# Kernel optimization log

Hardware: AMD Instinct MI355X
Metric: run time of the kernel (lower is better)

Reference implementation:

```python
import jax, jax.numpy as jnp
import numpy as np

EMBED_DIM = 768
NUM_HEADS = 12
HEAD_DIM = EMBED_DIM // NUM_HEADS
SCALE = HEAD_DIM ** -0.5


def setup_inputs() -> dict:
    key = jax.random.key(0)
    k1, k2, k3, k4, k5 = jax.random.split(key, 5)
    B, T = 8, 1024
    init = 0.02
    return {
        "hidden_states": jax.random.normal(k1, (B, T, EMBED_DIM), dtype=jnp.float32),
        "qkv_w": jax.random.normal(k2, (EMBED_DIM, 3 * EMBED_DIM), dtype=jnp.float32) * init,
        "qkv_b": jnp.zeros((3 * EMBED_DIM,), dtype=jnp.float32),
        "proj_w": jax.random.normal(k3, (EMBED_DIM, EMBED_DIM), dtype=jnp.float32) * init,
        "proj_b": jnp.zeros((EMBED_DIM,), dtype=jnp.float32),
    }


def reference(hidden_states, qkv_w, qkv_b, proj_w, proj_b):
    B, T, E = hidden_states.shape
    # fused QKV projection: [B, T, 3E] -> [3, B, H, T, Dh]
    mixed = hidden_states @ qkv_w + qkv_b
    mixed = mixed.reshape(B, T, 3, NUM_HEADS, HEAD_DIM).transpose(2, 0, 3, 1, 4)
    q, k, v = mixed[0], mixed[1], mixed[2]
    # scores: [B, H, T, T]
    scores = jnp.einsum("bhqd,bhkd->bhqk", q, k) * SCALE
    probs = jax.nn.softmax(scores, axis=-1)
    # context: [B, T, H, Dh] -> [B, T, E]
    ctx = jnp.einsum("bhqk,bhkd->bqhd", probs, v).reshape(B, T, E)
    return ctx @ proj_w + proj_b
```

## Files before the change

### kernel.cpp

```cpp
#include <hip/hip_runtime.h>
#include <hip/hip_bf16.h>

#define B_ 8
#define T_ 1024
#define E_ 768
#define H_ 12
#define DH_ 64
#define E3_ 2304
#define M_ (B_ * T_)
#define SCALE_LOG2E 0.18033688011112042f

typedef __attribute__((ext_vector_type(8))) short short8;
typedef __attribute__((ext_vector_type(4))) float float4_;
typedef __attribute__((ext_vector_type(4))) unsigned short ushort4_;

__device__ __forceinline__ unsigned short f2bf(float f) {
    union { float f; unsigned int u; } v; v.f = f;
    unsigned int r = v.u + 0x7fffu + ((v.u >> 16) & 1u);
    return (unsigned short)(r >> 16);
}

__device__ __forceinline__ void gld_lds16(const unsigned short* g, unsigned short* l) {
    __builtin_amdgcn_global_load_lds(
        (const __attribute__((address_space(1))) void*)g,
        (__attribute__((address_space(3))) void*)l,
        16, 0, 0);
}

__global__ __launch_bounds__(256) void prep(const float* __restrict__ hs,
                                            const float* __restrict__ qkv_w,
                                            const float* __restrict__ proj_w,
                                            unsigned short* __restrict__ hs_bf,
                                            unsigned short* __restrict__ qkvwT,
                                            unsigned short* __restrict__ projwT) {
    __shared__ float tile[32][33];
    const int id = blockIdx.x;
    const int tid = threadIdx.x;
    if (id < 6144) {
        const int i = (id * 256 + tid) * 4;
        float4_ v = *(const float4_*)(hs + i);
        ushort4_ o;
        o.x = f2bf(v.x); o.y = f2bf(v.y); o.z = f2bf(v.z); o.w = f2bf(v.w);
        *(ushort4_*)(hs_bf + i) = o;
        return;
    }
    const float* W; unsigned short* Wt; int N, bx, by;
    if (id < 6144 + 1728) {
        const int t = id - 6144; W = qkv_w; Wt = qkvwT; N = E3_;
        bx = t % 72; by = t / 72;
    } else {
        const int t = id - 7872; W = proj_w; Wt = projwT; N = E_;
        bx = t % 24; by = t / 24;
    }
    const int k0 = by * 32, n0 = bx * 32;
    const int tx = tid & 31, ty = tid >> 5;
    for (int i = ty; i < 32; i += 8)
        tile[i][tx] = W[(size_t)(k0 + i) * N + n0 + tx];
    __syncthreads();
    for (int i = ty; i < 32; i += 8)
        Wt[(size_t)(n0 + i) * E_ + k0 + tx] = f2bf(tile[tx][i]);
}

template <int STORE_MODE>
__global__ __launch_bounds__(256) void gemm_mfma(const unsigned short* __restrict__ A,
                                                 const unsigned short* __restrict__ Wt,
                                                 const float* __restrict__ bias,
                                                 void* __restrict__ Cout,
                                                 unsigned short* __restrict__ Vt,
                                                 int M, int N, int K) {
    __shared__ __align__(16) unsigned short Al[2][128 * 32];
    __shared__ __align__(16) unsigned short Wl[2][128 * 32];

    const int tid = threadIdx.x;
    const int lane = tid & 63;
    const int w = tid >> 6;

    const int id = blockIdx.x;
    const int xcd = id & 7;
    const int slot = id >> 3;
    const int bx = slot >> 3;
    const int by = xcd * 8 + (slot & 7);
    const int bm = by * 128;
    const int bn = bx * 128;

    const int wm = (w >> 1) * 64;
    const int wn = (w & 1) * 64;
    const int quad = lane >> 4;
    const int l16 = lane & 15;

    const int srow = w * 32 + (lane >> 2);
    const int schunk = (lane & 3) * 8;
    const int sbase = w * 32 * 32 + lane * 8;

    const unsigned short* ga = A + (size_t)(bm + srow) * K + schunk;
    const unsigned short* gw = Wt + (size_t)(bn + srow) * K + schunk;

    float4_ acc[4][4] = {};

    gld_lds16(ga, &Al[0][sbase]);
    gld_lds16(ga + (size_t)16 * K, &Al[0][sbase + 512]);
    gld_lds16(gw, &Wl[0][sbase]);
    gld_lds16(gw + (size_t)16 * K, &Wl[0][sbase + 512]);

    const int NI = K >> 5;
    for (int i = 0; i < NI; ++i) {
        const int cur = i & 1;
        __syncthreads();
        if (i + 1 < NI) {
            const unsigned short* ga2 = ga + (size_t)(i + 1) * 32;
            const unsigned short* gw2 = gw + (size_t)(i + 1) * 32;
            const int nxt = cur ^ 1;
            gld_lds16(ga2, &Al[nxt][sbase]);
            gld_lds16(ga2 + (size_t)16 * K, &Al[nxt][sbase + 512]);
            gld_lds16(gw2, &Wl[nxt][sbase]);
            gld_lds16(gw2 + (size_t)16 * K, &Wl[nxt][sbase + 512]);
        }
        short8 af[4], bf[4];
#pragma unroll
        for (int mt = 0; mt < 4; ++mt)
            af[mt] = *(const short8*)(&Al[cur][(wm + mt * 16 + l16) * 32 + quad * 8]);
#pragma unroll
        for (int nt = 0; nt < 4; ++nt)
            bf[nt] = *(const short8*)(&Wl[cur][(wn + nt * 16 + l16) * 32 + quad * 8]);
#pragma unroll
        for (int mt = 0; mt < 4; ++mt)
#pragma unroll
            for (int nt = 0; nt < 4; ++nt)
                acc[mt][nt] = __builtin_amdgcn_mfma_f32_16x16x32_bf16(af[mt], bf[nt],
                                                                      acc[mt][nt], 0, 0, 0);
    }

    if (STORE_MODE == 2 && bn >= 1536) {
        const int b = bm >> 10;
        const int tloc = (bm & 1023) + wm;
#pragma unroll
        for (int nt = 0; nt < 4; ++nt) {
            const int col = bn + wn + nt * 16 + l16;
            const int n = col - 1536;
            const int h = n >> 6, d = n & 63;
            const float bv = bias[col];
            const size_t vrow = (size_t)((b * H_ + h) * 64 + d) * T_;
#pragma unroll
            for (int mt = 0; mt < 4; ++mt) {
                ushort4_ pk;
                pk.x = f2bf(acc[mt][nt][0] + bv);
                pk.y = f2bf(acc[mt][nt][1] + bv);
                pk.z = f2bf(acc[mt][nt][2] + bv);
                pk.w = f2bf(acc[mt][nt][3] + bv);
                *(ushort4_*)(Vt + vrow + tloc + mt * 16 + quad * 4) = pk;
            }
        }
    } else {
        const float qs = (STORE_MODE == 2 && bn < 768) ? SCALE_LOG2E : 1.0f;
#pragma unroll
        for (int nt = 0; nt < 4; ++nt) {
            const int col = bn + wn + nt * 16 + l16;
            const float bv = bias[col];
#pragma unroll
            for (int mt = 0; mt < 4; ++mt) {
#pragma unroll
                for (int i = 0; i < 4; ++i) {
                    const int row = bm + wm + mt * 16 + quad * 4 + i;
                    const float v = (acc[mt][nt][i] + bv) * qs;
                    if (STORE_MODE >= 1)
                        ((unsigned short*)Cout)[(size_t)row * N + col] = f2bf(v);
                    else
                        ((float*)Cout)[(size_t)row * N + col] = v;
                }
            }
        }
    }
}

__global__ __launch_bounds__(256) void attn_mfma(const unsigned short* __restrict__ mixed,
                                                 const unsigned short* __restrict__ Vt,
                                                 unsigned short* __restrict__ ctx) {
    const int bh = blockIdx.x;
    const int b = bh / H_;
    const int h = bh % H_;
    const int q0 = blockIdx.y * 128;
    const int tid = threadIdx.x;
    const int lane = tid & 63;
    const int w = tid >> 6;
    const int quad = lane >> 4;
    const int l16 = lane & 15;

    __shared__ __align__(16) unsigned short Kl[8 * 520];
    __shared__ __align__(16) unsigned short Vl[8 * 520];
    __shared__ __align__(16) unsigned short Pl[4][32 * 72];
    unsigned short* pw = &Pl[w][0];

    short8 qf[2][2];
#pragma unroll
    for (int hh = 0; hh < 2; ++hh) {
        const size_t qrow = (size_t)(b * T_ + q0 + w * 32 + hh * 16 + l16) * E3_ + h * 64;
        qf[hh][0] = *(const short8*)(mixed + qrow + quad * 8);
        qf[hh][1] = *(const short8*)(mixed + qrow + 32 + quad * 8);
    }

    float4_ o[2][4] = {};
    float lps[2] = {0.0f, 0.0f};

    const size_t kbase = (size_t)(b * T_) * E3_ + E_ + h * 64;
    const size_t vtb = (size_t)bh * 64 * T_;

    const int srow = tid >> 3;
    const int sc = tid & 7;

    for (int kv0 = 0; kv0 < T_; kv0 += 64) {
        short8 k1 = *(const short8*)(mixed + kbase + (size_t)(kv0 + srow) * E3_ + sc * 8);
        short8 k2 = *(const short8*)(mixed + kbase + (size_t)(kv0 + srow + 32) * E3_ + sc * 8);
        short8 v1 = *(const short8*)(Vt + vtb + (size_t)srow * T_ + kv0 + sc * 8);
        short8 v2 = *(const short8*)(Vt + vtb + (size_t)(srow + 32) * T_ + kv0 + sc * 8);
        __syncthreads();
        *(short8*)(&Kl[sc * 520 + srow * 8]) = k1;
        *(short8*)(&Kl[sc * 520 + (srow + 32) * 8]) = k2;
        *(short8*)(&Vl[sc * 520 + srow * 8]) = v1;
        *(short8*)(&Vl[sc * 520 + (srow + 32) * 8]) = v2;
        __syncthreads();

        float4_ st[2][4];
#pragma unroll
        for (int nt = 0; nt < 4; ++nt) {
            const int key = nt * 16 + l16;
            short8 kf0 = *(const short8*)(&Kl[quad * 520 + key * 8]);
            short8 kf1 = *(const short8*)(&Kl[(4 + quad) * 520 + key * 8]);
#pragma unroll
            for (int hh = 0; hh < 2; ++hh) {
                float4_ z = {};
                z = __builtin_amdgcn_mfma_f32_16x16x32_bf16(kf0, qf[hh][0], z, 0, 0, 0);
                st[hh][nt] = __builtin_amdgcn_mfma_f32_16x16x32_bf16(kf1, qf[hh][1], z, 0, 0, 0);
            }
        }

#pragma unroll
        for (int hh = 0; hh < 2; ++hh) {
#pragma unroll
            for (int nt = 0; nt < 4; ++nt) {
                ushort4_ pk;
                float p0 = exp2f(st[hh][nt][0]);
                float p1 = exp2f(st[hh][nt][1]);
                float p2 = exp2f(st[hh][nt][2]);
                float p3 = exp2f(st[hh][nt][3]);
                pk.x = f2bf(p0); pk.y = f2bf(p1); pk.z = f2bf(p2); pk.w = f2bf(p3);
                lps[hh] += (p0 + p1) + (p2 + p3);
                *(ushort4_*)(&pw[(hh * 16 + l16) * 72 + nt * 16 + quad * 4]) = pk;
            }
        }

        short8 pf[2][2];
#pragma unroll
        for (int hh = 0; hh < 2; ++hh) {
            pf[hh][0] = *(const short8*)(&pw[(hh * 16 + l16) * 72 + quad * 8]);
            pf[hh][1] = *(const short8*)(&pw[(hh * 16 + l16) * 72 + 32 + quad * 8]);
        }

#pragma unroll
        for (int dt = 0; dt < 4; ++dt) {
            const int d = dt * 16 + l16;
            short8 vf0 = *(const short8*)(&Vl[quad * 520 + d * 8]);
            short8 vf1 = *(const short8*)(&Vl[(4 + quad) * 520 + d * 8]);
#pragma unroll
            for (int hh = 0; hh < 2; ++hh) {
                o[hh][dt] = __builtin_amdgcn_mfma_f32_16x16x32_bf16(pf[hh][0], vf0, o[hh][dt], 0, 0, 0);
                o[hh][dt] = __builtin_amdgcn_mfma_f32_16x16x32_bf16(pf[hh][1], vf1, o[hh][dt], 0, 0, 0);
            }
        }
    }

#pragma unroll
    for (int hh = 0; hh < 2; ++hh) {
        float l = lps[hh];
        l += __shfl_xor(l, 16, 64);
        l += __shfl_xor(l, 32, 64);
        float4_ inv;
#pragma unroll
        for (int i = 0; i < 4; ++i)
            inv[i] = 1.0f / __shfl(l, quad * 4 + i, 16);
#pragma unroll
        for (int dt = 0; dt < 4; ++dt) {
#pragma unroll
            for (int i = 0; i < 4; ++i) {
                const float v = o[hh][dt][i] * inv[i];
                const size_t row = (size_t)(b * T_ + q0 + w * 32 + hh * 16 + quad * 4 + i);
                ctx[row * E_ + h * 64 + dt * 16 + l16] = f2bf(v);
            }
        }
    }
}

extern "C" void kernel_launch(void* const* d_in, const int* in_sizes, int n_in,
                              void* d_out, int out_size, void* d_ws, size_t ws_size,
                              hipStream_t stream) {
    const float* hs     = (const float*)d_in[0];
    const float* qkv_w  = (const float*)d_in[1];
    const float* qkv_b  = (const float*)d_in[2];
    const float* proj_w = (const float*)d_in[3];
    const float* proj_b = (const float*)d_in[4];
    float* out = (float*)d_out;

    unsigned short* hs_bf  = (unsigned short*)d_ws;
    unsigned short* qkvwT  = hs_bf + (size_t)M_ * E_;
    unsigned short* projwT = qkvwT + (size_t)E3_ * E_;
    unsigned short* mixed  = projwT + (size_t)E_ * E_;
    unsigned short* Vt     = mixed + (size_t)M_ * E3_;
    unsigned short* ctx    = hs_bf;

    prep<<<8448, 256, 0, stream>>>(hs, qkv_w, proj_w, hs_bf, qkvwT, projwT);

    gemm_mfma<2><<<(E3_ / 128) * (M_ / 128), 256, 0, stream>>>(hs_bf, qkvwT, qkv_b,
                                                               (void*)mixed, Vt, M_, E3_, E_);
    attn_mfma<<<dim3(B_ * H_, T_ / 128), 256, 0, stream>>>(mixed, Vt, ctx);
    gemm_mfma<0><<<(E_ / 128) * (M_ / 128), 256, 0, stream>>>(ctx, projwT, proj_b,
                                                              (void*)out, nullptr, M_, E_, E_);
}
```

Before: 214.8 us.

## Add 256x256-tile pipelined MFMA GEMM for the QKV projection

```diff
diff --git a/kernel.cpp b/kernel.cpp
--- a/kernel.cpp
+++ b/kernel.cpp
@@ -130,38 +130,186 @@
                                                                       acc[mt][nt], 0, 0, 0);
     }
 
+    {
+        const float qs = 1.0f;
+#pragma unroll
+        for (int nt = 0; nt < 4; ++nt) {
+            const int col = bn + wn + nt * 16 + l16;
+            const float bv = bias[col];
+#pragma unroll
+            for (int mt = 0; mt < 4; ++mt) {
+#pragma unroll
+                for (int i = 0; i < 4; ++i) {
+                    const int row = bm + wm + mt * 16 + quad * 4 + i;
+                    const float v = (acc[mt][nt][i] + bv) * qs;
+                    if (STORE_MODE >= 1)
+                        ((unsigned short*)Cout)[(size_t)row * N + col] = f2bf(v);
+                    else
+                        ((float*)Cout)[(size_t)row * N + col] = v;
+                }
+            }
+        }
+    }
+    (void)Vt;
+}
+
+template <int STORE_MODE>
+__global__ __launch_bounds__(512, 2) void gemm256(const unsigned short* __restrict__ A,
+                                                  const unsigned short* __restrict__ Wt,
+                                                  const float* __restrict__ bias,
+                                                  void* __restrict__ Cout,
+                                                  unsigned short* __restrict__ Vt,
+                                                  int M, int N, int K) {
+    __shared__ __align__(16) unsigned short lds[65536];
+
+    const int tid = threadIdx.x;
+    const int lane = tid & 63;
+    const int w = tid >> 6;
+    const int quad = lane >> 4;
+    const int l16 = lane & 15;
+
+    const int id = blockIdx.x;
+    const int xcd = id & 7;
+    const int slot = id >> 3;
+    const int bx = slot >> 2;
+    const int byl = slot & 3;
+    const int bm = (xcd * 4 + byl) * 256;
+    const int bn = bx * 256;
+
+    const int rb = tid >> 3;
+    const int csw = (((tid & 7) ^ (rb & 7)) << 3);
+    const unsigned short* ga = A + (size_t)(bm + rb) * K + csw;
+    const unsigned short* gb = Wt + (size_t)(bn + (rb & 31) + ((rb >> 5) & 1) * 64) * K + csw;
+    unsigned short* ldst = lds + tid * 8;
+
+#define STA(p, h, s, kt) gld_lds16(ga + ((size_t)((h) * 128 + (s) * 64) * K + (kt) * 64), \
+                                   ldst + ((p) * 2 + (h)) * 8192 + (s) * 4096)
+#define STB(p, h, s, kt) gld_lds16(gb + ((size_t)((h) * 128 + (s) * 32) * K + (kt) * 64), \
+                                   ldst + 32768 + ((p) * 2 + (h)) * 8192 + (s) * 4096)
+
+    const int sw0 = ((quad ^ (l16 & 7)) << 3);
+    const int sw1 = (((quad + 4) ^ (l16 & 7)) << 3);
+    const unsigned short* rdA = lds + (w >> 2) * 8192 + l16 * 64;
+    const unsigned short* rdB = lds + 32768 + ((w & 3) >> 1) * 8192 + ((w & 1) * 32 + l16) * 64;
+
+    short8 aF[4][2], bF0[2][2], bF1[2][2];
+    float4_ acc[8][4] = {};
+
+#define LDA(p, mh) { \
+    const unsigned short* _a = rdA + (p) * 16384 + (mh) * 4096; \
+    _Pragma("unroll") for (int mt = 0; mt < 4; ++mt) { \
+        aF[mt][0] = *(const short8*)(_a + mt * 1024 + sw0); \
+        aF[mt][1] = *(const short8*)(_a + mt * 1024 + sw1); } }
+#define LDB(dst, p, nh) { \
+    const unsigned short* _b = rdB + (p) * 16384 + (nh) * 4096; \
+    dst[0][0] = *(const short8*)(_b + sw0); \
+    dst[0][1] = *(const short8*)(_b + sw1); \
+    dst[1][0] = *(const short8*)(_b + 1024 + sw0); \
+    dst[1][1] = *(const short8*)(_b + 1024 + sw1); }
+
+#define MMA(mh, nh, BF) \
+    __builtin_amdgcn_s_barrier(); \
+    asm volatile("s_waitcnt lgkmcnt(0)" ::: "memory"); \
+    __builtin_amdgcn_sched_barrier(0); \
+    __builtin_amdgcn_s_setprio(1); \
+    _Pragma("unroll") for (int mt = 0; mt < 4; ++mt) \
+    _Pragma("unroll") for (int nt = 0; nt < 2; ++nt) { \
+        acc[(mh) * 4 + mt][(nh) * 2 + nt] = __builtin_amdgcn_mfma_f32_16x16x32_bf16( \
+            aF[mt][0], BF[nt][0], acc[(mh) * 4 + mt][(nh) * 2 + nt], 0, 0, 0); \
+        acc[(mh) * 4 + mt][(nh) * 2 + nt] = __builtin_amdgcn_mfma_f32_16x16x32_bf16( \
+            aF[mt][1], BF[nt][1], acc[(mh) * 4 + mt][(nh) * 2 + nt], 0, 0, 0); } \
+    __builtin_amdgcn_s_setprio(0);
+
+#define WAITV8 asm volatile("s_waitcnt vmcnt(8)" ::: "memory"); __builtin_amdgcn_s_barrier();
+
+    STA(0, 0, 0, 0); STA(0, 1, 0, 0);
+    STB(0, 0, 0, 0); STB(0, 1, 0, 0);
+    STB(0, 0, 1, 0); STB(0, 1, 1, 0);
+    STA(0, 0, 1, 0); STA(0, 1, 1, 0);
+    STA(1, 0, 0, 1); STA(1, 1, 0, 1);
+    STB(1, 0, 0, 1); STB(1, 1, 0, 1);
+    STB(1, 0, 1, 1); STB(1, 1, 1, 1);
+    asm volatile("s_waitcnt vmcnt(6)" ::: "memory");
+    __builtin_amdgcn_s_barrier();
+
+    const int NJ = K >> 7;
+#pragma unroll 1
+    for (int j = 0; j < NJ; ++j) {
+        const int t1 = 2 * j + 1, t2 = 2 * j + 2, t3 = 2 * j + 3;
+        const bool st = (j < NJ - 1);
+
+        LDA(0, 0); LDB(bF0, 0, 0);
+        STA(1, 0, 1, t1); STA(1, 1, 1, t1);
+        MMA(0, 0, bF0);
+        WAITV8;
+        LDB(bF1, 0, 1);
+        if (st) { STA(0, 0, 0, t2); STA(0, 1, 0, t2); }
+        MMA(0, 1, bF1);
+        WAITV8;
+        LDA(0, 1);
+        if (st) { STB(0, 0, 0, t2); STB(0, 1, 0, t2); }
+        MMA(1, 0, bF0);
+        WAITV8;
+        if (st) { STB(0, 0, 1, t2); STB(0, 1, 1, t2); }
+        MMA(1, 1, bF1);
+        if (j == NJ - 1) asm volatile("s_waitcnt vmcnt(0)" ::: "memory");
+        else             asm volatile("s_waitcnt vmcnt(8)" ::: "memory");
+        __builtin_amdgcn_s_barrier();
+        LDA(1, 0); LDB(bF0, 1, 0);
+        if (st) { STA(0, 0, 1, t2); STA(0, 1, 1, t2); }
+        MMA(0, 0, bF0);
+        WAITV8;
+        LDB(bF1, 1, 1);
+        if (st) { STA(1, 0, 0, t3); STA(1, 1, 0, t3); }
+        MMA(0, 1, bF1);
+        WAITV8;
+        LDA(1, 1);
+        if (st) { STB(1, 0, 0, t3); STB(1, 1, 0, t3); }
+        MMA(1, 0, bF0);
+        WAITV8;
+        if (st) { STB(1, 0, 1, t3); STB(1, 1, 1, t3); }
+        MMA(1, 1, bF1);
+        WAITV8;
+    }
+#undef STA
+#undef STB
+#undef LDA
+#undef LDB
+#undef MMA
+#undef WAITV8
+
     if (STORE_MODE == 2 && bn >= 1536) {
         const int b = bm >> 10;
-        const int tloc = (bm & 1023) + wm;
-#pragma unroll
-        for (int nt = 0; nt < 4; ++nt) {
-            const int col = bn + wn + nt * 16 + l16;
+        const int tloc = (bm & 1023) + (w >> 2) * 128;
+#pragma unroll
+        for (int ni = 0; ni < 4; ++ni) {
+            const int col = bn + (w & 3) * 64 + (ni >> 1) * 32 + (ni & 1) * 16 + l16;
             const int n = col - 1536;
             const int h = n >> 6, d = n & 63;
             const float bv = bias[col];
             const size_t vrow = (size_t)((b * H_ + h) * 64 + d) * T_;
 #pragma unroll
-            for (int mt = 0; mt < 4; ++mt) {
+            for (int mi = 0; mi < 8; ++mi) {
                 ushort4_ pk;
-                pk.x = f2bf(acc[mt][nt][0] + bv);
-                pk.y = f2bf(acc[mt][nt][1] + bv);
-                pk.z = f2bf(acc[mt][nt][2] + bv);
-                pk.w = f2bf(acc[mt][nt][3] + bv);
-                *(ushort4_*)(Vt + vrow + tloc + mt * 16 + quad * 4) = pk;
+                pk.x = f2bf(acc[mi][ni][0] + bv);
+                pk.y = f2bf(acc[mi][ni][1] + bv);
+                pk.z = f2bf(acc[mi][ni][2] + bv);
+                pk.w = f2bf(acc[mi][ni][3] + bv);
+                *(ushort4_*)(Vt + vrow + tloc + (mi >> 2) * 64 + (mi & 3) * 16 + quad * 4) = pk;
             }
         }
     } else {
         const float qs = (STORE_MODE == 2 && bn < 768) ? SCALE_LOG2E : 1.0f;
 #pragma unroll
-        for (int nt = 0; nt < 4; ++nt) {
-            const int col = bn + wn + nt * 16 + l16;
+        for (int ni = 0; ni < 4; ++ni) {
+            const int col = bn + (w & 3) * 64 + (ni >> 1) * 32 + (ni & 1) * 16 + l16;
             const float bv = bias[col];
 #pragma unroll
-            for (int mt = 0; mt < 4; ++mt) {
+            for (int mi = 0; mi < 8; ++mi) {
 #pragma unroll
                 for (int i = 0; i < 4; ++i) {
-                    const int row = bm + wm + mt * 16 + quad * 4 + i;
-                    const float v = (acc[mt][nt][i] + bv) * qs;
+                    const int row = bm + (w >> 2) * 128 + (mi >> 2) * 64 + (mi & 3) * 16 + quad * 4 + i;
+                    const float v = (acc[mi][ni][i] + bv) * qs;
                     if (STORE_MODE >= 1)
                         ((unsigned short*)Cout)[(size_t)row * N + col] = f2bf(v);
                     else
@@ -308,8 +456,8 @@
 
     prep<<<8448, 256, 0, stream>>>(hs, qkv_w, proj_w, hs_bf, qkvwT, projwT);
 
-    gemm_mfma<2><<<(E3_ / 128) * (M_ / 128), 256, 0, stream>>>(hs_bf, qkvwT, qkv_b,
-                                                               (void*)mixed, Vt, M_, E3_, E_);
+    gemm256<2><<<(E3_ / 256) * (M_ / 256), 512, 0, stream>>>(hs_bf, qkvwT, qkv_b,
+                                                             (void*)mixed, Vt, M_, E3_, E_);
     attn_mfma<<<dim3(B_ * H_, T_ / 128), 256, 0, stream>>>(mixed, Vt, ctx);
     gemm_mfma<0><<<(E_ / 128) * (M_ / 128), 256, 0, stream>>>(ctx, projwT, proj_b,
                                                               (void*)out, nullptr, M_, E_, E_);
```

Measured after the change: 213.6 us. About the same (-0.5%).

## Replace QKV GEMM with 256x288-tile, XCD-aware, double-buffered swizzled MFMA kernel

Applied to the files above, without the earlier changes.

```diff
diff --git a/kernel.cpp b/kernel.cpp
--- a/kernel.cpp
+++ b/kernel.cpp
@@ -130,28 +130,7 @@
                                                                       acc[mt][nt], 0, 0, 0);
     }
 
-    if (STORE_MODE == 2 && bn >= 1536) {
-        const int b = bm >> 10;
-        const int tloc = (bm & 1023) + wm;
-#pragma unroll
-        for (int nt = 0; nt < 4; ++nt) {
-            const int col = bn + wn + nt * 16 + l16;
-            const int n = col - 1536;
-            const int h = n >> 6, d = n & 63;
-            const float bv = bias[col];
-            const size_t vrow = (size_t)((b * H_ + h) * 64 + d) * T_;
-#pragma unroll
-            for (int mt = 0; mt < 4; ++mt) {
-                ushort4_ pk;
-                pk.x = f2bf(acc[mt][nt][0] + bv);
-                pk.y = f2bf(acc[mt][nt][1] + bv);
-                pk.z = f2bf(acc[mt][nt][2] + bv);
-                pk.w = f2bf(acc[mt][nt][3] + bv);
-                *(ushort4_*)(Vt + vrow + tloc + mt * 16 + quad * 4) = pk;
-            }
-        }
-    } else {
-        const float qs = (STORE_MODE == 2 && bn < 768) ? SCALE_LOG2E : 1.0f;
+    {
 #pragma unroll
         for (int nt = 0; nt < 4; ++nt) {
             const int col = bn + wn + nt * 16 + l16;
@@ -161,11 +140,175 @@
 #pragma unroll
                 for (int i = 0; i < 4; ++i) {
                     const int row = bm + wm + mt * 16 + quad * 4 + i;
-                    const float v = (acc[mt][nt][i] + bv) * qs;
+                    const float v = acc[mt][nt][i] + bv;
                     if (STORE_MODE >= 1)
                         ((unsigned short*)Cout)[(size_t)row * N + col] = f2bf(v);
                     else
                         ((float*)Cout)[(size_t)row * N + col] = v;
+                }
+            }
+        }
+    }
+    (void)Vt;
+}
+
+__global__ __launch_bounds__(512, 2) void gemm288(const unsigned short* __restrict__ A,
+                                                  const unsigned short* __restrict__ Wt,
+                                                  const float* __restrict__ bias,
+                                                  unsigned short* __restrict__ mixedOut,
+                                                  unsigned short* __restrict__ Vt) {
+    const int K = 768;
+    const int NT = 12;
+    __shared__ __align__(16) unsigned short lds[70144];
+
+    const int tid = threadIdx.x;
+    const int lane = tid & 63;
+    const int w = tid >> 6;
+    const int quad = lane >> 4;
+    const int l16 = lane & 15;
+    const int wM = w >> 1;
+    const int wN = w & 1;
+
+    const int id = blockIdx.x;
+    const int xcd = id & 7;
+    const int slot = id >> 3;
+    const int bx = slot >> 2;
+    const int byl = slot & 3;
+    const int bm = (xcd * 4 + byl) * 256;
+    const int bn = bx * 288;
+
+    const int j4 = (w < 4) ? (w + 32) : 36;
+    int kk0 = ((w % 18) / 6) * 64 + w;
+    int kk1 = (((w + 8) % 18) / 6) * 64 + (w + 8);
+    int kk2 = (((w + 16) % 18) / 6) * 64 + (w + 16);
+    int kk3 = (((w + 24) % 18) / 6) * 64 + (w + 24);
+    int kk4 = (j4 >= 36) ? (3 * 64 + 36) : (((j4 % 18) / 6) * 64 + j4);
+#define CS_(a, b) { int _lo = min(a, b), _hi = max(a, b); a = _lo; b = _hi; }
+    CS_(kk0, kk1) CS_(kk3, kk4) CS_(kk2, kk4) CS_(kk2, kk3) CS_(kk1, kk4)
+    CS_(kk0, kk3) CS_(kk0, kk2) CS_(kk1, kk3) CS_(kk1, kk2)
+#undef CS_
+    const int b0 = kk0 & 63, b1 = kk1 & 63, b2 = kk2 & 63, b3 = kk3 & 63, b4 = kk4 & 63;
+
+    const int srcrow = lane >> 3;
+    const int ssw = ((lane & 7) ^ (srcrow & 7)) << 3;
+    const unsigned short* gaL = A + (size_t)(bm + srcrow) * K + ssw;
+    const unsigned short* gbL = Wt + (size_t)(bn + srcrow) * K + ssw;
+    unsigned short* ldsl = lds + lane * 8;
+
+    const int rsw0 = ((quad) ^ (l16 & 7)) << 3;
+    const int rsw1 = ((quad + 4) ^ (l16 & 7)) << 3;
+    const unsigned short* rdA = lds + (wM * 64 + l16) * 64;
+    const unsigned short* rdB = lds + 32768 + (wN * 144 + l16) * 64;
+
+    short8 aF[4][2], bF[3][2];
+    float4_ acc[4][9] = {};
+
+#define STA_(aj, toff, bufA) gld_lds16(gaL + (size_t)(aj) * 6144 + (toff), (bufA) + (aj) * 512)
+#define STB_(j, toff, bufB) { \
+    const int _j = (j); \
+    const unsigned short* _s = gbL + (size_t)(_j >= 36 ? 0 : _j) * 6144 + (toff); \
+    unsigned short* _d = (_j >= 36) ? (ldsl + 69632) : ((bufB) + _j * 512); \
+    gld_lds16(_s, _d); }
+
+#define LDA_(buf) { \
+    const unsigned short* _a = rdA + (buf) * 16384; \
+    aF[0][0] = *(const short8*)(_a + rsw0);        aF[0][1] = *(const short8*)(_a + rsw1); \
+    aF[1][0] = *(const short8*)(_a + 1024 + rsw0); aF[1][1] = *(const short8*)(_a + 1024 + rsw1); \
+    aF[2][0] = *(const short8*)(_a + 2048 + rsw0); aF[2][1] = *(const short8*)(_a + 2048 + rsw1); \
+    aF[3][0] = *(const short8*)(_a + 3072 + rsw0); aF[3][1] = *(const short8*)(_a + 3072 + rsw1); }
+
+#define LDB_(buf, nh) { \
+    const unsigned short* _b = rdB + (buf) * 18432 + (nh) * 3072; \
+    bF[0][0] = *(const short8*)(_b + rsw0);        bF[0][1] = *(const short8*)(_b + rsw1); \
+    bF[1][0] = *(const short8*)(_b + 1024 + rsw0); bF[1][1] = *(const short8*)(_b + 1024 + rsw1); \
+    bF[2][0] = *(const short8*)(_b + 2048 + rsw0); bF[2][1] = *(const short8*)(_b + 2048 + rsw1); }
+
+#define MMA_(nh) \
+    __builtin_amdgcn_s_setprio(1); \
+    _Pragma("unroll") for (int mt = 0; mt < 4; ++mt) \
+    _Pragma("unroll") for (int nt = 0; nt < 3; ++nt) { \
+        acc[mt][(nh) * 3 + nt] = __builtin_amdgcn_mfma_f32_16x16x32_bf16( \
+            aF[mt][0], bF[nt][0], acc[mt][(nh) * 3 + nt], 0, 0, 0); \
+        acc[mt][(nh) * 3 + nt] = __builtin_amdgcn_mfma_f32_16x16x32_bf16( \
+            aF[mt][1], bF[nt][1], acc[mt][(nh) * 3 + nt], 0, 0, 0); } \
+    __builtin_amdgcn_s_setprio(0);
+
+#define BARRIER_ __builtin_amdgcn_s_barrier()
+#define WLGKM0_ { asm volatile("s_waitcnt lgkmcnt(0)" ::: "memory"); __builtin_amdgcn_sched_barrier(0); }
+#define WVM3_ asm volatile("s_waitcnt vmcnt(3)" ::: "memory")
+#define WVM0_ asm volatile("s_waitcnt vmcnt(0)" ::: "memory")
+
+    {
+        unsigned short* bufA = ldsl;
+        unsigned short* bufB = ldsl + 32768;
+        STA_(w, 0, bufA); STA_(w + 8, 0, bufA); STA_(w + 16, 0, bufA); STA_(w + 24, 0, bufA);
+        STB_(b0, 0, bufB); STB_(b1, 0, bufB); STB_(b2, 0, bufB); STB_(b3, 0, bufB); STB_(b4, 0, bufB);
+    }
+    WVM3_; BARRIER_;
+
+#pragma unroll 1
+    for (int t = 0; t < NT - 1; ++t) {
+        const int buf = t & 1;
+        const int toff = (t + 1) * 64;
+        unsigned short* bufA = ldsl + (buf ^ 1) * 16384;
+        unsigned short* bufB = ldsl + 32768 + (buf ^ 1) * 18432;
+
+        LDA_(buf); LDB_(buf, 0);
+        STA_(w, toff, bufA); STA_(w + 8, toff, bufA); STA_(w + 16, toff, bufA);
+        BARRIER_; WLGKM0_; MMA_(0);
+        WVM3_; BARRIER_;
+        LDB_(buf, 1);
+        STA_(w + 24, toff, bufA); STB_(b0, toff, bufB); STB_(b1, toff, bufB);
+        BARRIER_; WLGKM0_; MMA_(1);
+        WVM3_; BARRIER_;
+        LDB_(buf, 2);
+        STB_(b2, toff, bufB); STB_(b3, toff, bufB); STB_(b4, toff, bufB);
+        BARRIER_; WLGKM0_; MMA_(2);
+        WVM3_; BARRIER_;
+    }
+    {
+        LDA_(1); LDB_(1, 0);
+        BARRIER_; WLGKM0_; MMA_(0);
+        WVM0_; BARRIER_;
+        LDB_(1, 1);
+        BARRIER_; WLGKM0_; MMA_(1);
+        BARRIER_;
+        LDB_(1, 2);
+        BARRIER_; WLGKM0_; MMA_(2);
+    }
+#undef STA_
+#undef STB_
+#undef LDA_
+#undef LDB_
+#undef MMA_
+
+    const int bb = bm >> 10;
+    const int tloc = (bm & 1023) + wM * 64;
+#pragma unroll
+    for (int ntg = 0; ntg < 9; ++ntg) {
+        const int col = bn + wN * 144 + ntg * 16 + l16;
+        const float bv = bias[col];
+        if (col >= 1536) {
+            const int n = col - 1536;
+            const int h = n >> 6, d = n & 63;
+            const size_t vrow = (size_t)((bb * H_ + h) * 64 + d) * T_;
+#pragma unroll
+            for (int mt = 0; mt < 4; ++mt) {
+                ushort4_ pk;
+                pk.x = f2bf(acc[mt][ntg][0] + bv);
+                pk.y = f2bf(acc[mt][ntg][1] + bv);
+                pk.z = f2bf(acc[mt][ntg][2] + bv);
+                pk.w = f2bf(acc[mt][ntg][3] + bv);
+                *(ushort4_*)(Vt + vrow + tloc + mt * 16 + quad * 4) = pk;
+            }
+        } else {
+            const float qs = (col < 768) ? SCALE_LOG2E : 1.0f;
+#pragma unroll
+            for (int mt = 0; mt < 4; ++mt) {
+#pragma unroll
+                for (int i = 0; i < 4; ++i) {
+                    const int row = bm + wM * 64 + mt * 16 + quad * 4 + i;
+                    mixedOut[(size_t)row * E3_ + col] = f2bf((acc[mt][ntg][i] + bv) * qs);
                 }
             }
         }
@@ -308,8 +451,7 @@
 
     prep<<<8448, 256, 0, stream>>>(hs, qkv_w, proj_w, hs_bf, qkvwT, projwT);
 
-    gemm_mfma<2><<<(E3_ / 128) * (M_ / 128), 256, 0, stream>>>(hs_bf, qkvwT, qkv_b,
-                                                               (void*)mixed, Vt, M_, E3_, E_);
+    gemm288<<<256, 512, 0, stream>>>(hs_bf, qkvwT, qkv_b, mixed, Vt);
     attn_mfma<<<dim3(B_ * H_, T_ / 128), 256, 0, stream>>>(mixed, Vt, ctx);
     gemm_mfma<0><<<(E_ / 128) * (M_ / 128), 256, 0, stream>>>(ctx, projwT, proj_b,
                                                               (void*)out, nullptr, M_, E_, E_);
```

Result: faster. 191.8 us (-10.7%).
